# Kernel tuning notes

Measured on AMD Instinct MI355X. Metric: run time of the kernel, lower is better.

## Reference

```python
import jax, jax.numpy as jnp
import numpy as np

B, S, H = 2, 2048, 2048           # batch, seq_len, hidden_size
NH, HD = 16, 128                  # num_heads, head_dim
ROPE_THETA = 10000.0


def _rope_cos_sin(seq_len, head_dim, dtype):
    # standard rotary embedding tables: [seq, head_dim]
    inv_freq = 1.0 / (ROPE_THETA ** (jnp.arange(0, head_dim, 2, dtype=jnp.float32) / head_dim))
    t = jnp.arange(seq_len, dtype=jnp.float32)
    freqs = jnp.einsum('s,d->sd', t, inv_freq)          # [S, HD/2]
    emb = jnp.concatenate([freqs, freqs], axis=-1)      # [S, HD]
    return jnp.cos(emb).astype(dtype), jnp.sin(emb).astype(dtype)


def _rotate_half(x):
    x1, x2 = jnp.split(x, 2, axis=-1)
    return jnp.concatenate([-x2, x1], axis=-1)


def _apply_rope(x, cos, sin):
    # x: [B, S, NH, HD]; cos/sin: [S, HD]
    return x * cos[None, :, None, :] + _rotate_half(x) * sin[None, :, None, :]


def setup_inputs() -> dict:
    key = jax.random.key(0)
    ks = jax.random.split(key, 10)
    hidden_states = jax.random.normal(ks[0], (B, S, H), dtype=jnp.float32)
    # causal mask: 1.0 where attention is disallowed (k > q), matching mask * -1e9 usage
    mask = jnp.triu(jnp.ones((S, S), dtype=jnp.float32), k=1)[None, None, :, :]
    mask = jnp.broadcast_to(mask, (B, 1, S, S))
    xav = 1.0 / np.sqrt(H)
    Wq = jax.random.uniform(ks[1], (H, NH, HD), jnp.float32, -xav, xav)
    Wk = jax.random.uniform(ks[2], (H, NH, HD), jnp.float32, -xav, xav)
    Wv = jax.random.uniform(ks[3], (H, NH, HD), jnp.float32, -xav, xav)
    Wo = jax.random.uniform(ks[4], (NH, HD, H), jnp.float32, -xav, xav)
    bq = jnp.zeros((NH, HD), jnp.float32)
    bk = jnp.zeros((NH, HD), jnp.float32)
    bv = jnp.zeros((NH, HD), jnp.float32)
    bo = jnp.zeros((H,), jnp.float32)
    return {"hidden_states": hidden_states, "mask": mask, "Wq": Wq, "bq": bq,
            "Wk": Wk, "bk": bk, "Wv": Wv, "bv": bv, "Wo": Wo, "bo": bo}


def reference(hidden_states, mask, Wq, bq, Wk, bk, Wv, bv, Wo, bo):
    dtype = hidden_states.dtype
    scale = 1.0 / jnp.sqrt(jnp.asarray(HD, dtype))
    # q/k/v projections: DenseGeneral hidden -> (heads, head_dim)
    q = jnp.einsum('bsh,bhd->bsnd'.replace('bhd', 'hnd'), hidden_states, Wq) + bq  # [B,S,NH,HD]
    k = jnp.einsum('bsh,hnd->bsnd', hidden_states, Wk) + bk
    v = jnp.einsum('bsh,hnd->bsnd', hidden_states, Wv) + bv
    cos, sin = _rope_cos_sin(hidden_states.shape[1], HD, dtype)
    q = _apply_rope(q, cos, sin)
    k = _apply_rope(k, cos, sin)
    # [B,NH,S,HD]
    q, k, v = (x.transpose(0, 2, 1, 3) for x in (q, k, v))
    attn_scores = jnp.einsum('bhqd,bhkd->bhqk', q, k) * scale
    attn_scores = attn_scores + mask * (-1e9)           # mask broadcasts over heads
    probs = jax.nn.softmax(attn_scores, axis=-1)
    attn_output = jnp.einsum('bhqk,bhkd->bhqd', probs, v)
    attn_output = attn_output.transpose(0, 2, 1, 3)      # [B,S,NH,HD]
    return jnp.einsum('bsnd,ndh->bsh', attn_output, Wo) + bo
```

## Files before the change

### kernel.cpp

```cpp
#include <hip/hip_runtime.h>
#include <hip/hip_bf16.h>

#define B_ 2
#define S_ 2048
#define H_ 2048
#define NH_ 16
#define HD_ 128
#define M_ (B_*S_)

typedef unsigned short u16;
typedef unsigned int u32;
typedef __attribute__((ext_vector_type(8))) short bhalf8_t;
typedef __attribute__((ext_vector_type(4))) float fx4_t;

__device__ __forceinline__ float bf2f(u16 v) {
    unsigned u = ((unsigned)v) << 16;
    return __builtin_bit_cast(float, u);
}
__device__ __forceinline__ u16 f2bf(float f) {
    unsigned u = __builtin_bit_cast(unsigned, f);
    unsigned r = u + 0x7fffu + ((u >> 16) & 1u);
    return (u16)(r >> 16);
}
__device__ __forceinline__ u16 f2bf_trunc(float f) {
    return (u16)(__builtin_bit_cast(unsigned, f) >> 16);
}
__device__ __forceinline__ void gload_lds16(const u16* g, u16* l) {
    __builtin_amdgcn_global_load_lds(
        (const __attribute__((address_space(1))) u32*)g,
        (__attribute__((address_space(3))) u32*)l, 16, 0, 0);
}
#define ASM_BAR()   __asm__ volatile("s_barrier" ::: "memory")
#define WAIT_VM0()  __asm__ volatile("s_waitcnt vmcnt(0)" ::: "memory")
#define WAIT_LGKM0() __asm__ volatile("s_waitcnt lgkmcnt(0)" ::: "memory")

__global__ __launch_bounds__(256) void cvt_bf16_k(const float* __restrict__ in,
                                                  u16* __restrict__ out) {
    int i = blockIdx.x * 256 + threadIdx.x;
    float4 v = ((const float4*)in)[i];
    ushort4 o;
    o.x = f2bf(v.x); o.y = f2bf(v.y); o.z = f2bf(v.z); o.w = f2bf(v.w);
    ((ushort4*)out)[i] = o;
}

__global__ __launch_bounds__(256) void transpose_cvt4_k(const float* __restrict__ s0,
                                                        const float* __restrict__ s1,
                                                        const float* __restrict__ s2,
                                                        const float* __restrict__ s3,
                                                        u16* __restrict__ out) {
    const float* in = blockIdx.z == 0 ? s0 : blockIdx.z == 1 ? s1
                    : blockIdx.z == 2 ? s2 : s3;
    u16* dst = out + (size_t)blockIdx.z * H_ * H_;
    __shared__ u16 tile[64][65];
    int k0 = blockIdx.y * 64, n0 = blockIdx.x * 64;
    int t = threadIdx.x;
    for (int i = 0; i < 16; i++) {
        int idx = t + i * 256;
        int r = idx >> 6, c = idx & 63;
        tile[r][c] = f2bf(in[(size_t)(k0 + r) * H_ + n0 + c]);
    }
    __syncthreads();
    for (int i = 0; i < 16; i++) {
        int idx = t + i * 256;
        int r = idx >> 6, c = idx & 63;
        dst[(size_t)(n0 + r) * H_ + k0 + c] = tile[c][r];
    }
}

__global__ __launch_bounds__(512, 2) void gemm_qkv8(const u16* __restrict__ A,
                                                    const u16* __restrict__ Bt,
                                                    const float* __restrict__ bq,
                                                    const float* __restrict__ bk,
                                                    const float* __restrict__ bv,
                                                    u16* __restrict__ qh,
                                                    u16* __restrict__ kh,
                                                    u16* __restrict__ vT) {
    const int Ksz = H_;
    __shared__ u16 sm8[4 * 16384];
    int t = threadIdx.x;
    int wave = t >> 6, lane = t & 63;
    int lr = lane & 15, lq = lane >> 4;
    int m0 = blockIdx.y * 256, n0 = blockIdx.x * 256;
    int wm = (wave >> 2) * 128, wn = (wave & 3) * 64;

    fx4_t acc[8][4];
#pragma unroll
    for (int i = 0; i < 8; i++)
        for (int j = 0; j < 4; j++)
            acc[i][j] = (fx4_t){0.f, 0.f, 0.f, 0.f};

    auto stageA = [&](int buf, int k0) {
        u16* dst = sm8 + buf * 16384;
#pragma unroll
        for (int i = 0; i < 4; i++) {
            int c = t + i * 512;
            int r = c >> 3, g = (c & 7) ^ (r & 7);
            gload_lds16(&A[(size_t)(m0 + r) * Ksz + k0 + g * 8], dst + (size_t)c * 8);
        }
    };
    auto stageB = [&](int buf, int k0) {
        u16* dst = sm8 + 32768 + buf * 16384;
#pragma unroll
        for (int i = 0; i < 4; i++) {
            int c = t + i * 512;
            int r = c >> 3, g = (c & 7) ^ (r & 7);
            gload_lds16(&Bt[(size_t)(n0 + r) * Ksz + k0 + g * 8], dst + (size_t)c * 8);
        }
    };

    const int NT = Ksz / 64;
    stageA(0, 0);
    stageB(0, 0);
    WAIT_VM0();
    ASM_BAR();

    for (int kt = 0; kt < NT; kt++) {
        int cur = kt & 1;
        const u16* Ab = sm8 + cur * 16384;
        const u16* Bb = sm8 + 32768 + cur * 16384;
        bhalf8_t bfr[8];

#pragma unroll
        for (int p = 0; p < 4; p++) {
            if (p == 0) {
#pragma unroll
                for (int nj = 0; nj < 4; nj++)
                    for (int ks = 0; ks < 2; ks++) {
                        int row = wn + nj * 16 + lr;
                        bfr[nj * 2 + ks] = *(const bhalf8_t*)
                            &Bb[(((size_t)row << 3) + ((ks * 4 + lq) ^ (lr & 7))) * 8];
                    }
            }
            bhalf8_t afr[2][2];
#pragma unroll
            for (int mi2 = 0; mi2 < 2; mi2++)
                for (int ks = 0; ks < 2; ks++) {
                    int row = wm + (p * 2 + mi2) * 16 + lr;
                    afr[mi2][ks] = *(const bhalf8_t*)
                        &Ab[(((size_t)row << 3) + ((ks * 4 + lq) ^ (lr & 7))) * 8];
                }
            if (kt + 1 < NT) {
                if (p == 0) stageA(cur ^ 1, (kt + 1) * 64);
                else if (p == 1) stageB(cur ^ 1, (kt + 1) * 64);
            }
            if (p == 3) WAIT_VM0();
            ASM_BAR();
            WAIT_LGKM0();
            __builtin_amdgcn_sched_barrier(0);
            __builtin_amdgcn_s_setprio(1);
#pragma unroll
            for (int mi2 = 0; mi2 < 2; mi2++)
                for (int nj = 0; nj < 4; nj++)
                    for (int ks = 0; ks < 2; ks++)
                        acc[p * 2 + mi2][nj] = __builtin_amdgcn_mfma_f32_16x16x32_bf16(
                            afr[mi2][ks], bfr[nj * 2 + ks], acc[p * 2 + mi2][nj], 0, 0, 0);
            __builtin_amdgcn_s_setprio(0);
            ASM_BAR();
        }
    }

    int which = n0 >> 11;
    const float* bias = which == 0 ? bq : which == 1 ? bk : bv;
#pragma unroll
    for (int mi = 0; mi < 8; mi++)
#pragma unroll
        for (int nj = 0; nj < 4; nj++) {
            int row0 = m0 + wm + mi * 16 + lq * 4;
            int cc = (n0 & 2047) + wn + nj * 16 + lr;
            float bvv = bias[cc];
            int bb = row0 >> 11, s = row0 & 2047;
            int hh = cc >> 7, d = cc & 127;
            if (which == 2) {
                ushort4 w;
                w.x = f2bf(acc[mi][nj][0] + bvv);
                w.y = f2bf(acc[mi][nj][1] + bvv);
                w.z = f2bf(acc[mi][nj][2] + bvv);
                w.w = f2bf(acc[mi][nj][3] + bvv);
                *(ushort4*)&vT[(((size_t)bb * NH_ + hh) * HD_ + d) * S_ + s] = w;
            } else {
                u16* dst = (which == 0 ? qh : kh);
                for (int r = 0; r < 4; r++)
                    dst[(((size_t)bb * NH_ + hh) * S_ + s + r) * HD_ + d] =
                        f2bf(acc[mi][nj][r] + bvv);
            }
        }
}

__global__ __launch_bounds__(256) void gemm_out(const u16* __restrict__ A,
                                                const u16* __restrict__ Bt,
                                                const float* __restrict__ bias,
                                                float* __restrict__ C) {
    const int Ksz = H_, Nsz = H_;
    __shared__ u16 As[128 * 64];
    __shared__ u16 Bs[128 * 64];
    int t = threadIdx.x;
    int wave = t >> 6, lane = t & 63;
    int lr = lane & 15, lq = lane >> 4;
    int m0 = blockIdx.y * 128, n0 = blockIdx.x * 128;
    int wm = (wave >> 1) * 64, wn = (wave & 1) * 64;

    fx4_t acc[4][4];
    for (int i = 0; i < 4; i++)
        for (int j = 0; j < 4; j++)
            acc[i][j] = (fx4_t){0.f, 0.f, 0.f, 0.f};

    for (int k0 = 0; k0 < Ksz; k0 += 64) {
        for (int i = 0; i < 4; i++) {
            int c = t + i * 256;
            int r = c >> 3, g = (c & 7) ^ (r & 7);
            gload_lds16(&A[(size_t)(m0 + r) * Ksz + k0 + g * 8], As + (size_t)c * 8);
            gload_lds16(&Bt[(size_t)(n0 + r) * Ksz + k0 + g * 8], Bs + (size_t)c * 8);
        }
        __syncthreads();
        for (int ds = 0; ds < 2; ds++) {
            bhalf8_t a[4], b[4];
            int cs = (ds * 4 + lq) ^ (lr & 7);
            for (int i = 0; i < 4; i++)
                a[i] = *(const bhalf8_t*)&As[(((wm + i * 16 + lr) << 3) + cs) * 8];
            for (int j = 0; j < 4; j++)
                b[j] = *(const bhalf8_t*)&Bs[(((wn + j * 16 + lr) << 3) + cs) * 8];
            for (int i = 0; i < 4; i++)
                for (int j = 0; j < 4; j++)
                    acc[i][j] = __builtin_amdgcn_mfma_f32_16x16x32_bf16(a[i], b[j], acc[i][j], 0, 0, 0);
        }
        __syncthreads();
    }
    for (int i = 0; i < 4; i++)
        for (int j = 0; j < 4; j++) {
            int row0 = m0 + wm + i * 16 + lq * 4;
            int col = n0 + wn + j * 16 + lr;
            float bvv = bias[col];
            for (int r = 0; r < 4; r++)
                C[(size_t)(row0 + r) * Nsz + col] = acc[i][j][r] + bvv;
        }
}

__global__ __launch_bounds__(256) void rope_k(u16* __restrict__ q, u16* __restrict__ k) {
    const float scale2 = 0.08838834764831845f * 1.44269504f;
    int idx = blockIdx.x * 256 + threadIdx.x;
    int i = idx & 63;
    int s = (idx >> 6) & 2047;
    int h = (idx >> 17) & 15;
    int b = idx >> 21;
    float inv = exp2f((float)i * (-13.287712379549449f / 64.0f));
    float ang = (float)s * inv;
    float sn, c;
    sincosf(ang, &sn, &c);
    size_t base = (((size_t)b * NH_ + h) * S_ + s) * HD_ + i;
    {
        float x1 = bf2f(q[base]), x2 = bf2f(q[base + 64]);
        q[base]      = f2bf((x1 * c - x2 * sn) * scale2);
        q[base + 64] = f2bf((x2 * c + x1 * sn) * scale2);
    }
    {
        float x1 = bf2f(k[base]), x2 = bf2f(k[base + 64]);
        k[base]      = f2bf(x1 * c - x2 * sn);
        k[base + 64] = f2bf(x2 * c + x1 * sn);
    }
}

#define PROW2 40
__global__ __launch_bounds__(256, 2) void flash_k(const u16* __restrict__ qh,
                                                  const u16* __restrict__ kh,
                                                  const u16* __restrict__ vT,
                                                  u16* __restrict__ attn) {
    __shared__ u16 sm[2 * 8192 + 2 * 8192 + 4 * 32 * PROW2];
    u16* KsB = sm;
    u16* VsB = sm + 16384;
    u16* Ps  = sm + 32768;

    int t = threadIdx.x, wave = t >> 6, lane = t & 63;
    int lr = lane & 15, lq = lane >> 4;
    int h = blockIdx.y, b = blockIdx.z;
    int ti = (b == 0) ? ((int)gridDim.x - 1 - (int)blockIdx.x) : (int)blockIdx.x;
    int q0 = ti * 128;

    const u16* kbase = kh + ((size_t)b * NH_ + h) * S_ * HD_;
    const u16* vbase = vT + ((size_t)b * NH_ + h) * HD_ * S_;
    u16* Pw = Ps + wave * 32 * PROW2;

    bhalf8_t aq[2][4];
#pragma unroll
    for (int rg = 0; rg < 2; rg++) {
        const u16* qrow =
            qh + (((size_t)b * NH_ + h) * S_ + q0 + wave * 32 + rg * 16 + lr) * HD_;
#pragma unroll
        for (int ds = 0; ds < 4; ds++)
            aq[rg][ds] = *(const bhalf8_t*)&qrow[ds * 32 + lq * 8];
    }

    float m_i[2][4], l_i[2][4];
    fx4_t acc_o[2][8];
#pragma unroll
    for (int rg = 0; rg < 2; rg++)
        for (int r = 0; r < 4; r++) { m_i[rg][r] = -INFINITY; l_i[rg][r] = 0.f; }
#pragma unroll
    for (int rg = 0; rg < 2; rg++)
        for (int dt = 0; dt < 8; dt++) acc_o[rg][dt] = (fx4_t){0.f, 0.f, 0.f, 0.f};

    bhalf8_t bones;
#pragma unroll
    for (int j = 0; j < 8; j++) bones[j] = (short)0x3F80;

    auto stageK = [&](int buf, int k0) {
        u16* dst = KsB + buf * 8192;
#pragma unroll
        for (int i = 0; i < 4; i++) {
            int c = t + i * 256;
            int r = c >> 4, g = (c & 15) ^ (r & 15);
            gload_lds16(&kbase[(size_t)(k0 + r) * HD_ + g * 8], dst + (size_t)c * 8);
        }
    };
    auto stageV = [&](int buf, int k0) {
        u16* dst = VsB + buf * 8192;
#pragma unroll
        for (int i = 0; i < 4; i++) {
            int c = t + i * 256;
            int r = c >> 3, g = (c & 7) ^ (r & 7);
            gload_lds16(&vbase[(size_t)r * S_ + k0 + g * 8], dst + (size_t)c * 8);
        }
    };

    int nkb = q0 / 64 + 2;
    stageK(0, 0);
    stageV(0, 0);
    for (int kbi = 0; kbi < nkb; kbi++) {
        int cur = kbi & 1;
        int k0 = kbi * 64;
        __syncthreads();
        if (kbi + 1 < nkb) {
            stageK(cur ^ 1, k0 + 64);
            stageV(cur ^ 1, k0 + 64);
        }
        const u16* Kc = KsB + cur * 8192;
        const u16* Vc = VsB + cur * 8192;

        bool active = (k0 <= q0 + wave * 32 + 31);

        fx4_t sacc[2][4];
        float alpha[2][4];
        if (active) {
#pragma unroll
            for (int rg = 0; rg < 2; rg++)
                for (int nt = 0; nt < 4; nt++)
                    sacc[rg][nt] = (fx4_t){0.f, 0.f, 0.f, 0.f};
            __builtin_amdgcn_s_setprio(1);
#pragma unroll
            for (int nt = 0; nt < 4; nt++) {
                int r = nt * 16 + lr;
#pragma unroll
                for (int ds = 0; ds < 4; ds++) {
                    bhalf8_t bk = *(const bhalf8_t*)&Kc[((r << 4) + ((ds * 4 + lq) ^ lr)) * 8];
                    sacc[0][nt] = __builtin_amdgcn_mfma_f32_16x16x32_bf16(aq[0][ds], bk, sacc[0][nt], 0, 0, 0);
                    sacc[1][nt] = __builtin_amdgcn_mfma_f32_16x16x32_bf16(aq[1][ds], bk, sacc[1][nt], 0, 0, 0);
                }
            }
            __builtin_amdgcn_s_setprio(0);

            if (kbi >= nkb - 2) {
#pragma unroll
                for (int rg = 0; rg < 2; rg++)
                    for (int nt = 0; nt < 4; nt++)
                        for (int r = 0; r < 4; r++) {
                            int kpos = k0 + nt * 16 + lr;
                            int qpos = q0 + wave * 32 + rg * 16 + lq * 4 + r;
                            if (kpos > qpos) sacc[rg][nt][r] = -1e30f;
                        }
            }

#pragma unroll
            for (int rg = 0; rg < 2; rg++) {
                float rmax[4];
#pragma unroll
                for (int r = 0; r < 4; r++)
                    rmax[r] = fmaxf(fmaxf(sacc[rg][0][r], sacc[rg][1][r]),
                                    fmaxf(sacc[rg][2][r], sacc[rg][3][r]));
#pragma unroll
                for (int off = 1; off < 16; off <<= 1)
                    for (int r = 0; r < 4; r++)
                        rmax[r] = fmaxf(rmax[r], __shfl_xor(rmax[r], off, 64));
#pragma unroll
                for (int r = 0; r < 4; r++) {
                    float mn = fmaxf(m_i[rg][r], rmax[r]);
                    alpha[rg][r] = exp2f(m_i[rg][r] - mn);
                    m_i[rg][r] = mn;
#pragma unroll
                    for (int nt = 0; nt < 4; nt++)
                        sacc[rg][nt][r] = exp2f(sacc[rg][nt][r] - mn);
                    l_i[rg][r] *= alpha[rg][r];
                }
#pragma unroll
                for (int dt = 0; dt < 8; dt++)
                    for (int r = 0; r < 4; r++) acc_o[rg][dt][r] *= alpha[rg][r];
            }

            fx4_t ls[2];
            ls[0] = (fx4_t){0.f, 0.f, 0.f, 0.f};
            ls[1] = (fx4_t){0.f, 0.f, 0.f, 0.f};
#pragma unroll
            for (int p = 0; p < 2; p++) {
#pragma unroll
                for (int rg = 0; rg < 2; rg++)
                    for (int nt2 = 0; nt2 < 2; nt2++)
                        for (int r = 0; r < 4; r++)
                            Pw[(rg * 16 + lq * 4 + r) * PROW2 + nt2 * 16 + lr] =
                                f2bf_trunc(sacc[rg][p * 2 + nt2][r]);
                __asm__ volatile("s_waitcnt lgkmcnt(0)" ::: "memory");
                bhalf8_t ap0 = *(const bhalf8_t*)&Pw[lr * PROW2 + lq * 8];
                bhalf8_t ap1 = *(const bhalf8_t*)&Pw[(16 + lr) * PROW2 + lq * 8];
                __builtin_amdgcn_s_setprio(1);
#pragma unroll
                for (int dt = 0; dt < 8; dt++) {
                    int r = dt * 16 + lr;
                    bhalf8_t bv = *(const bhalf8_t*)&Vc[((r << 3) + ((p * 4 + lq) ^ (lr & 7))) * 8];
                    acc_o[0][dt] = __builtin_amdgcn_mfma_f32_16x16x32_bf16(ap0, bv, acc_o[0][dt], 0, 0, 0);
                    acc_o[1][dt] = __builtin_amdgcn_mfma_f32_16x16x32_bf16(ap1, bv, acc_o[1][dt], 0, 0, 0);
                }
                ls[0] = __builtin_amdgcn_mfma_f32_16x16x32_bf16(ap0, bones, ls[0], 0, 0, 0);
                ls[1] = __builtin_amdgcn_mfma_f32_16x16x32_bf16(ap1, bones, ls[1], 0, 0, 0);
                __builtin_amdgcn_s_setprio(0);
            }
#pragma unroll
            for (int rg = 0; rg < 2; rg++)
                for (int r = 0; r < 4; r++) l_i[rg][r] += ls[rg][r];
        }
    }

#pragma unroll
    for (int rg = 0; rg < 2; rg++) {
        float rl[4];
#pragma unroll
        for (int r = 0; r < 4; r++) rl[r] = 1.f / l_i[rg][r];
#pragma unroll
        for (int dt = 0; dt < 8; dt++)
            for (int r = 0; r < 4; r++) {
                size_t row = (size_t)(b * S_ + q0 + wave * 32 + rg * 16 + lq * 4 + r);
                attn[(row * NH_ + h) * HD_ + dt * 16 + lr] = f2bf(acc_o[rg][dt][r] * rl[r]);
            }
    }
}

extern "C" void kernel_launch(void* const* d_in, const int* in_sizes, int n_in,
                              void* d_out, int out_size, void* d_ws, size_t ws_size,
                              hipStream_t stream) {
    const float* hs = (const float*)d_in[0];
    const float* Wq = (const float*)d_in[2];
    const float* bq = (const float*)d_in[3];
    const float* Wk = (const float*)d_in[4];
    const float* bk = (const float*)d_in[5];
    const float* Wv = (const float*)d_in[6];
    const float* bv = (const float*)d_in[7];
    const float* Wo = (const float*)d_in[8];
    const float* bo = (const float*)d_in[9];
    float* out = (float*)d_out;

    u16* ws   = (u16*)d_ws;
    size_t WW = (size_t)H_ * H_;
    size_t AC = (size_t)M_ * H_;
    u16* hsb  = ws;
    u16* Wall = hsb + AC;
    u16* WoT  = Wall + 3 * WW;
    u16* qh   = WoT + WW;
    u16* kh   = qh + AC;
    u16* vT   = kh + AC;
    u16* attn = vT + AC;

    dim3 tb(256);

    cvt_bf16_k<<<dim3(AC / (256 * 4)), tb, 0, stream>>>(hs, hsb);

    transpose_cvt4_k<<<dim3(32, 32, 4), tb, 0, stream>>>(Wq, Wk, Wv, Wo, Wall);

    gemm_qkv8<<<dim3(3 * H_ / 256, M_ / 256), dim3(512), 0, stream>>>(hsb, Wall,
                                                                      bq, bk, bv,
                                                                      qh, kh, vT);

    rope_k<<<dim3((B_ * NH_ * S_ * 64) / 256), tb, 0, stream>>>(qh, kh);

    flash_k<<<dim3(S_ / 128, NH_, B_), tb, 0, stream>>>(qh, kh, vT, attn);

    gemm_out<<<dim3(H_ / 128, M_ / 128), tb, 0, stream>>>(attn, WoT, bo, out);
}
```

Before: 435.0 us.

## Use triple-buffered LDS pipeline with smaller M tile in QKV GEMM

```diff
diff --git a/kernel.cpp b/kernel.cpp
--- a/kernel.cpp
+++ b/kernel.cpp
@@ -30,8 +30,9 @@
         (const __attribute__((address_space(1))) u32*)g,
         (__attribute__((address_space(3))) u32*)l, 16, 0, 0);
 }
-#define ASM_BAR()   __asm__ volatile("s_barrier" ::: "memory")
-#define WAIT_VM0()  __asm__ volatile("s_waitcnt vmcnt(0)" ::: "memory")
+#define ASM_BAR()    __asm__ volatile("s_barrier" ::: "memory")
+#define WAIT_VM0()   __asm__ volatile("s_waitcnt vmcnt(0)" ::: "memory")
+#define WAIT_VM6()   __asm__ volatile("s_waitcnt vmcnt(6)" ::: "memory")
 #define WAIT_LGKM0() __asm__ volatile("s_waitcnt lgkmcnt(0)" ::: "memory")
 
 __global__ __launch_bounds__(256) void cvt_bf16_k(const float* __restrict__ in,
@@ -67,39 +68,40 @@
     }
 }
 
-__global__ __launch_bounds__(512, 2) void gemm_qkv8(const u16* __restrict__ A,
-                                                    const u16* __restrict__ Bt,
-                                                    const float* __restrict__ bq,
-                                                    const float* __restrict__ bk,
-                                                    const float* __restrict__ bv,
-                                                    u16* __restrict__ qh,
-                                                    u16* __restrict__ kh,
-                                                    u16* __restrict__ vT) {
+__global__ __launch_bounds__(512, 2) void gemm_qkv_tb(const u16* __restrict__ A,
+                                                      const u16* __restrict__ Bt,
+                                                      const float* __restrict__ bq,
+                                                      const float* __restrict__ bk,
+                                                      const float* __restrict__ bv,
+                                                      u16* __restrict__ qh,
+                                                      u16* __restrict__ kh,
+                                                      u16* __restrict__ vT) {
     const int Ksz = H_;
-    __shared__ u16 sm8[4 * 16384];
+    __shared__ u16 smA[3 * 8192];
+    __shared__ u16 smB[3 * 16384];
     int t = threadIdx.x;
     int wave = t >> 6, lane = t & 63;
     int lr = lane & 15, lq = lane >> 4;
-    int m0 = blockIdx.y * 256, n0 = blockIdx.x * 256;
-    int wm = (wave >> 2) * 128, wn = (wave & 3) * 64;
-
-    fx4_t acc[8][4];
-#pragma unroll
-    for (int i = 0; i < 8; i++)
+    int m0 = blockIdx.y * 128, n0 = blockIdx.x * 256;
+    int wm = (wave >> 2) * 64, wn = (wave & 3) * 64;
+
+    fx4_t acc[4][4];
+#pragma unroll
+    for (int i = 0; i < 4; i++)
         for (int j = 0; j < 4; j++)
             acc[i][j] = (fx4_t){0.f, 0.f, 0.f, 0.f};
 
     auto stageA = [&](int buf, int k0) {
-        u16* dst = sm8 + buf * 16384;
-#pragma unroll
-        for (int i = 0; i < 4; i++) {
+        u16* dst = smA + buf * 8192;
+#pragma unroll
+        for (int i = 0; i < 2; i++) {
             int c = t + i * 512;
             int r = c >> 3, g = (c & 7) ^ (r & 7);
             gload_lds16(&A[(size_t)(m0 + r) * Ksz + k0 + g * 8], dst + (size_t)c * 8);
         }
     };
     auto stageB = [&](int buf, int k0) {
-        u16* dst = sm8 + 32768 + buf * 16384;
+        u16* dst = smB + buf * 16384;
 #pragma unroll
         for (int i = 0; i < 4; i++) {
             int c = t + i * 512;
@@ -109,60 +111,77 @@
     };
 
     const int NT = Ksz / 64;
-    stageA(0, 0);
-    stageB(0, 0);
-    WAIT_VM0();
+    stageA(0, 0);  stageB(0, 0);
+    stageA(1, 64); stageB(1, 64);
+    WAIT_VM6();
     ASM_BAR();
 
     for (int kt = 0; kt < NT; kt++) {
-        int cur = kt & 1;
-        const u16* Ab = sm8 + cur * 16384;
-        const u16* Bb = sm8 + 32768 + cur * 16384;
+        int cur = kt % 3;
+        const u16* Ab = smA + cur * 8192;
+        const u16* Bb = smB + cur * 16384;
         bhalf8_t bfr[8];
-
-#pragma unroll
-        for (int p = 0; p < 4; p++) {
-            if (p == 0) {
-#pragma unroll
-                for (int nj = 0; nj < 4; nj++)
-                    for (int ks = 0; ks < 2; ks++) {
-                        int row = wn + nj * 16 + lr;
-                        bfr[nj * 2 + ks] = *(const bhalf8_t*)
-                            &Bb[(((size_t)row << 3) + ((ks * 4 + lq) ^ (lr & 7))) * 8];
-                    }
-            }
-            bhalf8_t afr[2][2];
-#pragma unroll
-            for (int mi2 = 0; mi2 < 2; mi2++)
-                for (int ks = 0; ks < 2; ks++) {
-                    int row = wm + (p * 2 + mi2) * 16 + lr;
-                    afr[mi2][ks] = *(const bhalf8_t*)
-                        &Ab[(((size_t)row << 3) + ((ks * 4 + lq) ^ (lr & 7))) * 8];
-                }
-            if (kt + 1 < NT) {
-                if (p == 0) stageA(cur ^ 1, (kt + 1) * 64);
-                else if (p == 1) stageB(cur ^ 1, (kt + 1) * 64);
-            }
-            if (p == 3) WAIT_VM0();
-            ASM_BAR();
-            WAIT_LGKM0();
-            __builtin_amdgcn_sched_barrier(0);
-            __builtin_amdgcn_s_setprio(1);
-#pragma unroll
-            for (int mi2 = 0; mi2 < 2; mi2++)
-                for (int nj = 0; nj < 4; nj++)
-                    for (int ks = 0; ks < 2; ks++)
-                        acc[p * 2 + mi2][nj] = __builtin_amdgcn_mfma_f32_16x16x32_bf16(
-                            afr[mi2][ks], bfr[nj * 2 + ks], acc[p * 2 + mi2][nj], 0, 0, 0);
-            __builtin_amdgcn_s_setprio(0);
-            ASM_BAR();
-        }
+        bhalf8_t afr[2][2];
+
+#pragma unroll
+        for (int nj = 0; nj < 4; nj++)
+            for (int ks = 0; ks < 2; ks++) {
+                int row = wn + nj * 16 + lr;
+                bfr[nj * 2 + ks] = *(const bhalf8_t*)
+                    &Bb[(((size_t)row << 3) + ((ks * 4 + lq) ^ (lr & 7))) * 8];
+            }
+#pragma unroll
+        for (int mi2 = 0; mi2 < 2; mi2++)
+            for (int ks = 0; ks < 2; ks++) {
+                int row = wm + mi2 * 16 + lr;
+                afr[mi2][ks] = *(const bhalf8_t*)
+                    &Ab[(((size_t)row << 3) + ((ks * 4 + lq) ^ (lr & 7))) * 8];
+            }
+        if (kt + 2 < NT) {
+            int nb = (kt + 2) % 3;
+            stageA(nb, (kt + 2) * 64);
+            stageB(nb, (kt + 2) * 64);
+        }
+        ASM_BAR();
+        WAIT_LGKM0();
+        __builtin_amdgcn_sched_barrier(0);
+        __builtin_amdgcn_s_setprio(1);
+#pragma unroll
+        for (int mi2 = 0; mi2 < 2; mi2++)
+            for (int nj = 0; nj < 4; nj++)
+                for (int ks = 0; ks < 2; ks++)
+                    acc[mi2][nj] = __builtin_amdgcn_mfma_f32_16x16x32_bf16(
+                        afr[mi2][ks], bfr[nj * 2 + ks], acc[mi2][nj], 0, 0, 0);
+        __builtin_amdgcn_s_setprio(0);
+        ASM_BAR();
+
+#pragma unroll
+        for (int mi2 = 0; mi2 < 2; mi2++)
+            for (int ks = 0; ks < 2; ks++) {
+                int row = wm + (2 + mi2) * 16 + lr;
+                afr[mi2][ks] = *(const bhalf8_t*)
+                    &Ab[(((size_t)row << 3) + ((ks * 4 + lq) ^ (lr & 7))) * 8];
+            }
+        if (kt + 2 < NT) WAIT_VM6();
+        else            WAIT_VM0();
+        ASM_BAR();
+        WAIT_LGKM0();
+        __builtin_amdgcn_sched_barrier(0);
+        __builtin_amdgcn_s_setprio(1);
+#pragma unroll
+        for (int mi2 = 0; mi2 < 2; mi2++)
+            for (int nj = 0; nj < 4; nj++)
+                for (int ks = 0; ks < 2; ks++)
+                    acc[2 + mi2][nj] = __builtin_amdgcn_mfma_f32_16x16x32_bf16(
+                        afr[mi2][ks], bfr[nj * 2 + ks], acc[2 + mi2][nj], 0, 0, 0);
+        __builtin_amdgcn_s_setprio(0);
+        ASM_BAR();
     }
 
     int which = n0 >> 11;
     const float* bias = which == 0 ? bq : which == 1 ? bk : bv;
 #pragma unroll
-    for (int mi = 0; mi < 8; mi++)
+    for (int mi = 0; mi < 4; mi++)
 #pragma unroll
         for (int nj = 0; nj < 4; nj++) {
             int row0 = m0 + wm + mi * 16 + lq * 4;
@@ -471,9 +490,9 @@
 
     transpose_cvt4_k<<<dim3(32, 32, 4), tb, 0, stream>>>(Wq, Wk, Wv, Wo, Wall);
 
-    gemm_qkv8<<<dim3(3 * H_ / 256, M_ / 256), dim3(512), 0, stream>>>(hsb, Wall,
-                                                                      bq, bk, bv,
-                                                                      qh, kh, vT);
+    gemm_qkv_tb<<<dim3(3 * H_ / 256, M_ / 128), dim3(512), 0, stream>>>(hsb, Wall,
+                                                                        bq, bk, bv,
+                                                                        qh, kh, vT);
 
     rope_k<<<dim3((B_ * NH_ * S_ * 64) / 256), tb, 0, stream>>>(qh, kh);
 
```

Result: no change. 441.3 us (+1.5%).
